# Optimization experiments

Measured on AMD Instinct MI355X. Metric: run time of the kernel, lower is better.

## Reference

```python
import jax, jax.numpy as jnp
import numpy as np

C = 256
N, H, W = 4, 64, 64


def _conv1x1(x, w, b):
    # 1x1 Conv2d == per-pixel linear: x [N,C,H,W], w [O,C], b [O]
    return jnp.einsum('nchw,oc->nohw', x, w) + b[None, :, None, None]


def setup_inputs() -> dict:
    key = jax.random.key(0)
    ks = jax.random.split(key, 9)
    inputs = jax.random.normal(ks[0], (N, C, H, W), dtype=jnp.float32)
    scale = 1.0 / np.sqrt(C)
    d = {'inputs': inputs}
    for i in range(4):
        d[f'w{i}'] = jax.random.normal(ks[1 + 2 * i], (C, C), dtype=jnp.float32) * scale
        d[f'b{i}'] = jax.random.normal(ks[2 + 2 * i], (C,), dtype=jnp.float32) * 0.01
    return d


def reference(inputs, w0, b0, w1, b1, w2, b2, w3, b3):
    n, c, h, w = inputs.shape
    hw = h * w
    # f_v, f_k, f_q: [N, HW, C] (NCHW conv output permuted to NHWC then flattened)
    f_v = _conv1x1(inputs, w0, b0).transpose(0, 2, 3, 1).reshape(n, hw, c)
    f_k = _conv1x1(inputs, w1, b1).transpose(0, 2, 3, 1).reshape(n, hw, c)
    f_q = _conv1x1(inputs, w2, b2).transpose(0, 2, 3, 1).reshape(n, hw, c)
    # w[n,i,j] = <k_i, q_j> / HW   (no softmax)
    att = jnp.einsum('nid,njd->nij', f_k, f_q) / hw
    # f_r[n,j,c] = sum_i w[n,i,j] * v[n,i,c]  (matmul with w^T)
    f_r = jnp.einsum('nij,nic->njc', att, f_v)
    f_r = f_r.reshape(n, h, w, c).transpose(0, 3, 1, 2)  # back to NCHW
    return _conv1x1(f_r, w3, b3)
```

## Files before the change

### kernel.cpp

```cpp
#include <hip/hip_runtime.h>

#define NB 4
#define CD 256
#define HW 4096
#define KSG 16
#define CC (CD * CD)

typedef __attribute__((ext_vector_type(8))) short bf16x8;
typedef __attribute__((ext_vector_type(4))) float f32x4;

__device__ inline unsigned short f2bf(float x) {
  unsigned int u = __float_as_uint(x);
  unsigned int r = (u + 0x7FFFu + ((u >> 16) & 1u)) >> 16;
  return (unsigned short)r;
}
__device__ inline float bfhi(unsigned short h) {
  return __uint_as_float(((unsigned int)h) << 16);
}
__device__ __forceinline__ void gload16(const unsigned short* g, unsigned short* l) {
  __builtin_amdgcn_global_load_lds((const __attribute__((address_space(1))) void*)g,
                                   (__attribute__((address_space(3))) void*)l, 16, 0, 0);
}

template <int BOFF>
__device__ __forceinline__ void mfma_body(const unsigned short* sm, f32x4 acc[4][2]) {
  int t = threadIdx.x, lane = t & 63, wid = t >> 6;
  int wr = wid >> 2, wc = wid & 3;
  int lrow = lane & 15, lkb = lane >> 4;
#pragma unroll
  for (int ks2 = 0; ks2 < 2; ++ks2) {
    bf16x8 ah[4], al[4], bh[2], bl[2];
#pragma unroll
    for (int m = 0; m < 4; ++m) {
      int r = wr * 64 + m * 16 + lrow;
      int sw = ((ks2 * 4 + lkb) ^ (r & 7)) * 8;
      ah[m] = *(const bf16x8*)(sm + r * 64 + sw);
      al[m] = *(const bf16x8*)(sm + 8192 + r * 64 + sw);
    }
#pragma unroll
    for (int q = 0; q < 2; ++q) {
      int r = wc * 32 + q * 16 + lrow;
      int sw = ((ks2 * 4 + lkb) ^ (r & 7)) * 8;
      bh[q] = *(const bf16x8*)(sm + BOFF + r * 64 + sw);
      bl[q] = *(const bf16x8*)(sm + BOFF + 8192 + r * 64 + sw);
    }
#pragma unroll
    for (int m = 0; m < 4; ++m)
#pragma unroll
      for (int q = 0; q < 2; ++q) {
        acc[m][q] = __builtin_amdgcn_mfma_f32_16x16x32_bf16(ah[m], bh[q], acc[m][q], 0, 0, 0);
        acc[m][q] = __builtin_amdgcn_mfma_f32_16x16x32_bf16(ah[m], bl[q], acc[m][q], 0, 0, 0);
        acc[m][q] = __builtin_amdgcn_mfma_f32_16x16x32_bf16(al[m], bh[q], acc[m][q], 0, 0, 0);
      }
  }
}

__device__ __forceinline__ void mfma_nt_core(
    const unsigned short* __restrict__ pH, const unsigned short* __restrict__ pL,
    const unsigned short* __restrict__ qH, const unsigned short* __restrict__ qL,
    int i0, int j0, unsigned short* sm, f32x4 acc[4][2]) {
  int t = threadIdx.x;
  int lane = t & 63, wid = t >> 6;
  int tsel = wid >> 1;
  int gbase = (wid & 1) * 8;
  const unsigned short* bp2 = (tsel == 0) ? pH : (tsel == 1) ? pL : (tsel == 2) ? qH : qL;
  int tb = (tsel < 2) ? i0 : j0;
  int rsub = lane >> 3;
  int gc = (lane & 7) ^ rsub;
  unsigned short* ldsT = sm + tsel * 8192;
#pragma unroll
  for (int m = 0; m < 4; ++m)
#pragma unroll
    for (int q = 0; q < 2; ++q) acc[m][q] = (f32x4){0.f, 0.f, 0.f, 0.f};
  for (int k0 = 0; k0 < 256; k0 += 64) {
#pragma unroll
    for (int s = 0; s < 8; ++s) {
      int g = gbase + s;
      gload16(bp2 + (size_t)(tb + g * 8 + rsub) * CD + k0 + gc * 8, ldsT + g * 512);
    }
    __syncthreads();
    mfma_body<16384>(sm, acc);
    __syncthreads();
  }
}

template <bool DIAG, int NSTEP>
__device__ __forceinline__ void gram_core(const float* __restrict__ Xn, int i0, int j0,
                                          int kBegin, unsigned short* sm,
                                          f32x4 acc[4][2], float* __restrict__ psumRow) {
  int t = threadIdx.x;
  int r16 = t >> 4, k4 = (t & 15) * 4;
  int kg = k4 >> 3, kr = k4 & 7;
#pragma unroll
  for (int m = 0; m < 4; ++m)
#pragma unroll
    for (int q = 0; q < 2; ++q) acc[m][q] = (f32x4){0.f, 0.f, 0.f, 0.f};
  float ps[4] = {0.f, 0.f, 0.f, 0.f};
  float4 av[4], bv[4];
#pragma unroll
  for (int j = 0; j < 4; ++j) {
    av[j] = *(const float4*)(Xn + (size_t)(i0 + j * 32 + r16) * HW + kBegin + k4);
    if (!DIAG)
      bv[j] = *(const float4*)(Xn + (size_t)(j0 + j * 32 + r16) * HW + kBegin + k4);
  }
#pragma unroll
  for (int s = 0; s < NSTEP; ++s) {
    float4 av2[4], bv2[4];
    if (s < NSTEP - 1) {
#pragma unroll
      for (int j = 0; j < 4; ++j) {
        av2[j] = *(const float4*)(Xn + (size_t)(i0 + j * 32 + r16) * HW + kBegin +
                                  (s + 1) * 64 + k4);
        if (!DIAG)
          bv2[j] = *(const float4*)(Xn + (size_t)(j0 + j * 32 + r16) * HW + kBegin +
                                    (s + 1) * 64 + k4);
      }
    }
#pragma unroll
    for (int j = 0; j < 4; ++j) {
      int r = j * 32 + r16;
      int off = r * 64 + ((kg ^ (r & 7)) << 3) + kr;
      ushort4 h, l;
      h.x = f2bf(av[j].x); l.x = f2bf(av[j].x - bfhi(h.x));
      h.y = f2bf(av[j].y); l.y = f2bf(av[j].y - bfhi(h.y));
      h.z = f2bf(av[j].z); l.z = f2bf(av[j].z - bfhi(h.z));
      h.w = f2bf(av[j].w); l.w = f2bf(av[j].w - bfhi(h.w));
      *(ushort4*)(sm + off) = h;
      *(ushort4*)(sm + 8192 + off) = l;
      ps[j] += av[j].x + av[j].y + av[j].z + av[j].w;
      if (!DIAG) {
        h.x = f2bf(bv[j].x); l.x = f2bf(bv[j].x - bfhi(h.x));
        h.y = f2bf(bv[j].y); l.y = f2bf(bv[j].y - bfhi(h.y));
        h.z = f2bf(bv[j].z); l.z = f2bf(bv[j].z - bfhi(h.z));
        h.w = f2bf(bv[j].w); l.w = f2bf(bv[j].w - bfhi(h.w));
        *(ushort4*)(sm + 16384 + off) = h;
        *(ushort4*)(sm + 24576 + off) = l;
      }
    }
    __syncthreads();
    mfma_body<DIAG ? 0 : 16384>(sm, acc);
    __syncthreads();
    if (s < NSTEP - 1) {
#pragma unroll
      for (int j = 0; j < 4; ++j) {
        av[j] = av2[j];
        if (!DIAG) bv[j] = bv2[j];
      }
    }
  }
  if (psumRow) {
#pragma unroll
    for (int j = 0; j < 4; ++j) {
      float v = ps[j];
      v += __shfl_xor(v, 1); v += __shfl_xor(v, 2);
      v += __shfl_xor(v, 4); v += __shfl_xor(v, 8);
      if ((t & 15) == 0) psumRow[j * 32 + r16] = v;
    }
  }
}

__device__ __forceinline__ void stage_rowA(const float* __restrict__ W, int ld, int r0,
                                           int k0, unsigned short* dst) {
  int t = threadIdx.x;
  int r16 = t >> 4, k4 = (t & 15) * 4;
  int kg = k4 >> 3, kr = k4 & 7;
#pragma unroll
  for (int j = 0; j < 4; ++j) {
    int r = j * 32 + r16;
    float4 v = *(const float4*)(W + (size_t)(r0 + r) * ld + k0 + k4);
    int off = r * 64 + ((kg ^ (r & 7)) << 3) + kr;
    ushort4 h, l;
    h.x = f2bf(v.x); l.x = f2bf(v.x - bfhi(h.x));
    h.y = f2bf(v.y); l.y = f2bf(v.y - bfhi(h.y));
    h.z = f2bf(v.z); l.z = f2bf(v.z - bfhi(h.z));
    h.w = f2bf(v.w); l.w = f2bf(v.w - bfhi(h.w));
    *(ushort4*)(dst + off) = h;
    *(ushort4*)(dst + 8192 + off) = l;
  }
}

__device__ __forceinline__ void stage_colT(const float* __restrict__ W, int ld, int c0,
                                           int k0, unsigned short* dst) {
  int t = threadIdx.x;
#pragma unroll
  for (int ee = 0; ee < 8; ++ee) {
    int flat = ee * 512 + t;
    int c2 = flat >> 7, p = flat & 127;
    const float* src = W + (size_t)(k0 + 2 * c2) * ld + c0 + p;
    float xa = src[0], xb = src[ld];
    int c = 2 * c2;
    int off = p * 64 + ((((c >> 3)) ^ (p & 7)) << 3) + (c & 7);
    unsigned short ha = f2bf(xa), hb = f2bf(xb);
    ushort2 hv; hv.x = ha; hv.y = hb;
    ushort2 lv; lv.x = f2bf(xa - bfhi(ha)); lv.y = f2bf(xb - bfhi(hb));
    *(ushort2*)(dst + off) = hv;
    *(ushort2*)(dst + 8192 + off) = lv;
  }
}

__device__ __forceinline__ void mfma_body64(const unsigned short* sm, f32x4 acc[4]) {
  int t = threadIdx.x, lane = t & 63, wid = t >> 6;
  int wr = wid >> 2, wc = wid & 3;
  int lrow = lane & 15, lkb = lane >> 4;
#pragma unroll
  for (int ks2 = 0; ks2 < 2; ++ks2) {
    bf16x8 ah[4], al[4], bh, bl;
#pragma unroll
    for (int m = 0; m < 4; ++m) {
      int r = wr * 64 + m * 16 + lrow;
      int sw = ((ks2 * 4 + lkb) ^ (r & 7)) * 8;
      ah[m] = *(const bf16x8*)(sm + r * 64 + sw);
      al[m] = *(const bf16x8*)(sm + 8192 + r * 64 + sw);
    }
    {
      int r = wc * 16 + lrow;
      int sw = ((ks2 * 4 + lkb) ^ (r & 7)) * 8;
      bh = *(const bf16x8*)(sm + 16384 + r * 64 + sw);
      bl = *(const bf16x8*)(sm + 20480 + r * 64 + sw);
    }
#pragma unroll
    for (int m = 0; m < 4; ++m) {
      acc[m] = __builtin_amdgcn_mfma_f32_16x16x32_bf16(ah[m], bh, acc[m], 0, 0, 0);
      acc[m] = __builtin_amdgcn_mfma_f32_16x16x32_bf16(ah[m], bl, acc[m], 0, 0, 0);
      acc[m] = __builtin_amdgcn_mfma_f32_16x16x32_bf16(al[m], bh, acc[m], 0, 0, 0);
    }
  }
}

__device__ __forceinline__ void final_core64(const unsigned short* __restrict__ aH,
                                             const unsigned short* __restrict__ aL,
                                             const float* __restrict__ Xn, int i0, int j0,
                                             unsigned short* sm, f32x4 acc[4]) {
  int t = threadIdx.x, lane = t & 63, wid = t >> 6;
  const unsigned short* ap = (wid & 4) ? aL : aH;
  unsigned short* ldsA = sm + ((wid & 4) ? 8192 : 0);
  int rsub = lane >> 3;
  int gc = (lane & 7) ^ rsub;
  int gq = wid & 3;
#pragma unroll
  for (int m = 0; m < 4; ++m) acc[m] = (f32x4){0.f, 0.f, 0.f, 0.f};
  float xa[4], xb[4];
#pragma unroll
  for (int s2 = 0; s2 < 4; ++s2) {
    int g = gq * 4 + s2;
    gload16(ap + (size_t)(i0 + g * 8 + rsub) * CD + gc * 8, ldsA + g * 512);
  }
#pragma unroll
  for (int ee = 0; ee < 4; ++ee) {
    int flat = ee * 512 + t;
    int c2 = flat >> 6, p = flat & 63;
    const float* src = Xn + (size_t)(2 * c2) * HW + j0 + p;
    xa[ee] = src[0];
    xb[ee] = src[HW];
  }
#pragma unroll
  for (int s = 0; s < 4; ++s) {
#pragma unroll
    for (int ee = 0; ee < 4; ++ee) {
      int flat = ee * 512 + t;
      int c2 = flat >> 6, p = flat & 63;
      int c = 2 * c2;
      int off = p * 64 + ((((c >> 3)) ^ (p & 7)) << 3) + (c & 7);
      unsigned short ha = f2bf(xa[ee]), hb = f2bf(xb[ee]);
      ushort2 hv; hv.x = ha; hv.y = hb;
      ushort2 lv; lv.x = f2bf(xa[ee] - bfhi(ha)); lv.y = f2bf(xb[ee] - bfhi(hb));
      *(ushort2*)(sm + 16384 + off) = hv;
      *(ushort2*)(sm + 20480 + off) = lv;
    }
    float xa2[4], xb2[4];
    if (s < 3) {
#pragma unroll
      for (int ee = 0; ee < 4; ++ee) {
        int flat = ee * 512 + t;
        int c2 = flat >> 6, p = flat & 63;
        const float* src = Xn + (size_t)((s + 1) * 64 + 2 * c2) * HW + j0 + p;
        xa2[ee] = src[0];
        xb2[ee] = src[HW];
      }
    }
    __syncthreads();
    mfma_body64(sm, acc);
    __syncthreads();
    if (s < 3) {
#pragma unroll
      for (int s2 = 0; s2 < 4; ++s2) {
        int g = gq * 4 + s2;
        gload16(ap + (size_t)(i0 + g * 8 + rsub) * CD + (s + 1) * 64 + gc * 8,
                ldsA + g * 512);
      }
#pragma unroll
      for (int ee = 0; ee < 4; ++ee) { xa[ee] = xa2[ee]; xb[ee] = xb2[ee]; }
    }
  }
}

__device__ __forceinline__ void epi_store(f32x4 acc[4][2], float* smf, float* dst,
                                          int ld, const float* cvrow) {
  int t = threadIdx.x, lane = t & 63, wid = t >> 6;
  int wr = wid >> 2, wc = wid & 3;
#pragma unroll
  for (int m = 0; m < 4; ++m) {
    int rbase = wr * 64 + m * 16 + ((lane >> 4) << 2);
#pragma unroll
    for (int q = 0; q < 2; ++q) {
      int col = wc * 32 + q * 16 + (lane & 15);
#pragma unroll
      for (int e = 0; e < 4; ++e) {
        int row = rbase + e;
        smf[row * 128 + (col ^ ((row & 4) << 2))] = acc[m][q][e];
      }
    }
  }
  __syncthreads();
#pragma unroll
  for (int it = 0; it < 8; ++it) {
    int row = it * 16 + wid * 2 + (lane >> 5);
    int col = (lane & 31) * 4;
    float4 v = *(const float4*)&smf[row * 128 + (col ^ ((row & 4) << 2))];
    if (cvrow) {
      float cb = cvrow[row];
      v.x += cb; v.y += cb; v.z += cb; v.w += cb;
    }
    *(float4*)(dst + (size_t)row * ld + col) = v;
  }
}

__device__ __forceinline__ void epi_store64(f32x4 acc[4], float* smf, float* dst,
                                            const float* cvrow) {
  int t = threadIdx.x, lane = t & 63, wid = t >> 6;
  int wr = wid >> 2, wc = wid & 3;
#pragma unroll
  for (int m = 0; m < 4; ++m) {
    int rbase = wr * 64 + m * 16 + ((lane >> 4) << 2);
    int col = wc * 16 + (lane & 15);
#pragma unroll
    for (int e = 0; e < 4; ++e) {
      int row = rbase + e;
      smf[row * 64 + (col ^ ((row & 4) << 2))] = acc[m][e];
    }
  }
  __syncthreads();
#pragma unroll
  for (int it = 0; it < 4; ++it) {
    int slot = it * 512 + t;
    int row = slot >> 4, col = (slot & 15) * 4;
    float4 v = *(const float4*)&smf[row * 64 + (col ^ ((row & 4) << 2))];
    float cb = cvrow[row];
    v.x += cb; v.y += cb; v.z += cb; v.w += cb;
    *(float4*)(dst + (size_t)row * HW + col) = v;
  }
}

__global__ __launch_bounds__(512) void kB(
    const float* __restrict__ X, float* __restrict__ Gp, float* __restrict__ psum2,
    const float* __restrict__ w0, const float* __restrict__ w1,
    const float* __restrict__ w2, const float* __restrict__ w3,
    const float* __restrict__ b0, const float* __restrict__ b1,
    const float* __restrict__ b2, unsigned short* __restrict__ Eh,
    unsigned short* __restrict__ El, float* __restrict__ Et,
    unsigned short* __restrict__ Fth, unsigned short* __restrict__ Ftl,
    float* __restrict__ Ff, float* __restrict__ vp, float* __restrict__ bpv,
    float* __restrict__ dlt, float* __restrict__ scal1) {
  __shared__ __align__(16) unsigned short sm[32768];
  int x = blockIdx.x, t = threadIdx.x;
  if (x < 192) {
    int tile = x % 3;
    int z = x / 3;
    int n = z >> 4, ks = z & 15;
    const float* Xn = X + (size_t)n * CD * HW;
    f32x4 acc[4][2];
    if (tile == 1) {
      gram_core<false, 4>(Xn, 0, 128, ks * 256, sm, acc, nullptr);
      epi_store(acc, (float*)sm, Gp + ((size_t)ks * NB + n) * CC + 128, CD, nullptr);
    } else {
      int i0 = (tile == 2) ? 128 : 0;
      float* psRow = psum2 + ((size_t)n * KSG + ks) * 256 + i0;
      gram_core<true, 4>(Xn, i0, i0, ks * 256, sm, acc, psRow);
      epi_store(acc, (float*)sm,
                Gp + ((size_t)ks * NB + n) * CC + (size_t)i0 * CD + i0, CD, nullptr);
    }
  } else if (x < 200) {
    int e = x - 192;
    int zc = e >> 2, q = e & 3;
    int i0 = (q >> 1) * 128, j0 = (q & 1) * 128;
    f32x4 acc[4][2];
#pragma unroll
    for (int m = 0; m < 4; ++m)
#pragma unroll
      for (int qq = 0; qq < 2; ++qq) acc[m][qq] = (f32x4){0.f, 0.f, 0.f, 0.f};
    for (int s = 0; s < 4; ++s) {
      int k0 = s * 64;
      if (zc == 0) stage_rowA(w3, CD, i0, k0, sm);
      else stage_colT(w2, CD, i0, k0, sm);
      stage_colT(zc ? w1 : w0, CD, j0, k0, sm + 16384);
      __syncthreads();
      mfma_body<16384>(sm, acc);
      __syncthreads();
    }
    unsigned short* oh = zc ? Fth : Eh;
    unsigned short* ol = zc ? Ftl : El;
    float* tf = zc ? Ff : Et;
    int lane = t & 63, wid = t >> 6, wr = wid >> 2, wc = wid & 3;
#pragma unroll
    for (int m = 0; m < 4; ++m) {
      int row = i0 + wr * 64 + m * 16 + ((lane >> 4) << 2);
#pragma unroll
      for (int q2 = 0; q2 < 2; ++q2) {
        int col = j0 + wc * 32 + q2 * 16 + (lane & 15);
#pragma unroll
        for (int e2 = 0; e2 < 4; ++e2) {
          float v = acc[m][q2][e2];
          unsigned short hh = f2bf(v), ll = f2bf(v - bfhi(hh));
          oh[(size_t)(row + e2) * CD + col] = hh;
          ol[(size_t)(row + e2) * CD + col] = ll;
          tf[(size_t)col * CD + row + e2] = v;
        }
      }
    }
  } else {
    int task = x - 200;
    if (task < 8) {
      float* vin = (float*)sm;
      int seg = task & 3;
      const float* Wm = (task < 4) ? w1 : w2;
      const float* v = (task < 4) ? b2 : b1;
      float* dst = (task < 4) ? (vp + seg * CD) : (bpv + seg * CD);
      if (t < 64) vin[t] = v[seg * 64 + t];
      __syncthreads();
      if (t < 256) {
        float a = 0.f;
#pragma unroll 16
        for (int kk = 0; kk < 64; ++kk)
          a += Wm[(size_t)(seg * 64 + kk) * CD + t] * vin[kk];
        dst[t] = a;
      }
    } else if (task < 12) {
      int lane = t & 63, wv = t >> 6;
      float4 bvv = *(const float4*)(b0 + lane * 4);
#pragma unroll
      for (int i = 0; i < 8; ++i) {
        int o = (task - 8) * 64 + wv * 8 + i;
        float4 v = *(const float4*)(w3 + (size_t)o * CD + lane * 4);
        float a = v.x * bvv.x + v.y * bvv.y + v.z * bvv.z + v.w * bvv.w;
        a += __shfl_xor(a, 1);  a += __shfl_xor(a, 2);  a += __shfl_xor(a, 4);
        a += __shfl_xor(a, 8);  a += __shfl_xor(a, 16); a += __shfl_xor(a, 32);
        if (lane == 0) dlt[o] = a;
      }
    } else if (task == 12) {
      float* red = (float*)sm;
      if (t < 256) red[t] = b1[t] * b2[t];
      __syncthreads();
      for (int off = 128; off > 0; off >>= 1) {
        if (t < off) red[t] += red[t + off];
        __syncthreads();
      }
      if (t == 0) scal1[0] = red[0];
    }
  }
}

__global__ __launch_bounds__(512) void kC(
    const float* __restrict__ Gp, unsigned short* __restrict__ Gh,
    unsigned short* __restrict__ Gl, const float* __restrict__ psum2,
    const float* __restrict__ vp, const float* __restrict__ Ff,
    const float* __restrict__ Et, float* __restrict__ alp, float* __restrict__ gam,
    float* __restrict__ scal0) {
  __shared__ float smf[512];
  int b = blockIdx.x, t = threadIdx.x;
  if (b < 96) {
#pragma unroll
    for (int s = 0; s < 4; ++s) {
      int f = b * 2048 + s * 512 + t;
      int b2 = f >> 8, tt = f & 255;
      int quad = b2 >> 8, r = b2 & 255, n = r >> 6;
      int idx = (r & 63) * 256 + tt;
      int i = (idx >> 7) + ((quad == 2) ? 128 : 0);
      int j = (idx & 127) + ((quad >= 1) ? 128 : 0);
      float a = 0.f;
#pragma unroll
      for (int ks = 0; ks < KSG; ++ks)
        a += Gp[((size_t)ks * NB + n) * CC + (size_t)i * CD + j];
      size_t o = (size_t)n * CC + (size_t)i * CD + j;
      unsigned short hh = f2bf(a), ll = f2bf(a - bfhi(hh));
      Gh[o] = hh; Gl[o] = ll;
      if (quad == 1) {
        size_t o2 = (size_t)n * CC + (size_t)j * CD + i;
        Gh[o2] = hh; Gl[o2] = ll;
      }
    }
  } else {
    int n = b - 96;
    float* ss = smf;
    float* red = ss + 256;
    float a = 0.f;
    if (t < 256) {
#pragma unroll
      for (int ks = 0; ks < KSG; ++ks) a += psum2[((size_t)n * KSG + ks) * 256 + t];
      ss[t] = a;
      red[t] = a * (vp[t] + vp[CD + t] + vp[2 * CD + t] + vp[3 * CD + t]);
    }
    __syncthreads();
    for (int off = 128; off > 0; off >>= 1) {
      if (t < off) red[t] += red[t + off];
      __syncthreads();
    }
    if (t == 0) scal0[n] = red[0];
    if (t < 256) {
      float al = 0.f, ga = 0.f;
#pragma unroll 16
      for (int k = 0; k < CD; ++k) {
        float sk = ss[k];
        al += Ff[(size_t)k * CD + t] * sk;
        ga += Et[(size_t)k * CD + t] * sk;
      }
      alp[n * CD + t] = al;
      gam[n * CD + t] = ga;
    }
  }
}

__global__ __launch_bounds__(512) void kD1(
    const unsigned short* __restrict__ Eh, const unsigned short* __restrict__ El,
    const unsigned short* __restrict__ Gh, const unsigned short* __restrict__ Gl,
    unsigned short* __restrict__ Rh, unsigned short* __restrict__ Rl,
    const float* __restrict__ Et, const float* __restrict__ vp,
    const float* __restrict__ dlt, const float* __restrict__ gam,
    const float* __restrict__ scal0, const float* __restrict__ scal1,
    const float* __restrict__ b3, float* __restrict__ cv) {
  __shared__ __align__(16) unsigned short sm[32768];
  int b = blockIdx.x, t = threadIdx.x;
  if (b < 16) {
    int n = b >> 2, i0 = ((b >> 1) & 1) * 128, j0 = (b & 1) * 128;
    f32x4 acc[4][2];
    mfma_nt_core(Eh, El, Gh + (size_t)n * CC, Gl + (size_t)n * CC, i0, j0, sm, acc);
    int lane = t & 63, wid = t >> 6, wr = wid >> 2, wc = wid & 3;
#pragma unroll
    for (int m = 0; m < 4; ++m) {
      int row = i0 + wr * 64 + m * 16 + ((lane >> 4) << 2);
#pragma unroll
      for (int q = 0; q < 2; ++q) {
        int col = j0 + wc * 32 + q * 16 + (lane & 15);
#pragma unroll
        for (int e = 0; e < 4; ++e) {
          float v = acc[m][q][e];
          unsigned short hh = f2bf(v), ll = f2bf(v - bfhi(hh));
          Rh[(size_t)n * CC + (size_t)(row + e) * CD + col] = hh;
          Rl[(size_t)n * CC + (size_t)(row + e) * CD + col] = ll;
        }
      }
    }
  } else {
    int n = b - 16;
    float* vsh = (float*)sm;
    float* g1 = vsh + CD;
    if (t < CD) vsh[t] = vp[t] + vp[CD + t] + vp[2 * CD + t] + vp[3 * CD + t];
    __syncthreads();
    if (t < CD) {
      const unsigned short* GhN = Gh + (size_t)n * CC;
      const unsigned short* GlN = Gl + (size_t)n * CC;
      float a = 0.f;
#pragma unroll 8
      for (int k = 0; k < CD; ++k) {
        float g = bfhi(GhN[(size_t)k * CD + t]) + bfhi(GlN[(size_t)k * CD + t]);
        a += g * vsh[k];
      }
      g1[t] = a;
    }
    __syncthreads();
    if (t < CD) {
      float c2 = 0.f;
#pragma unroll 8
      for (int k = 0; k < CD; ++k) c2 += Et[(size_t)k * CD + t] * g1[k];
      cv[n * CD + t] = (c2 + scal0[n] * dlt[t] +
                        scal1[0] * (gam[n * CD + t] + (float)HW * dlt[t])) *
                           (1.0f / HW) +
                       b3[t];
    }
  }
}

__global__ __launch_bounds__(512) void kD2(
    const unsigned short* __restrict__ Rh, const unsigned short* __restrict__ Rl,
    const unsigned short* __restrict__ Fth, const unsigned short* __restrict__ Ftl,
    unsigned short* __restrict__ Athi, unsigned short* __restrict__ Atlo,
    const float* __restrict__ dlt, const float* __restrict__ alp,
    const float* __restrict__ gam, const float* __restrict__ bpv) {
  __shared__ __align__(16) unsigned short sm[32768];
  int b = blockIdx.x, t = threadIdx.x;
  int n = b >> 2, i0 = ((b >> 1) & 1) * 128, j0 = (b & 1) * 128;
  f32x4 acc[4][2];
  mfma_nt_core(Rh + (size_t)n * CC, Rl + (size_t)n * CC, Fth, Ftl, i0, j0, sm, acc);
  int lane = t & 63, wid = t >> 6, wr = wid >> 2, wc = wid & 3;
#pragma unroll
  for (int m = 0; m < 4; ++m) {
    int row = i0 + wr * 64 + m * 16 + ((lane >> 4) << 2);
#pragma unroll
    for (int q = 0; q < 2; ++q) {
      int col = j0 + wc * 32 + q * 16 + (lane & 15);
      float bj = bpv[col] + bpv[CD + col] + bpv[2 * CD + col] + bpv[3 * CD + col];
      float aj = alp[n * CD + col];
#pragma unroll
      for (int e = 0; e < 4; ++e) {
        float di = dlt[row + e], gi = gam[n * CD + row + e];
        float v = (acc[m][q][e] + di * aj + gi * bj) * (1.0f / HW) + di * bj;
        unsigned short hh = f2bf(v), ll = f2bf(v - bfhi(hh));
        Athi[(size_t)n * CC + (size_t)(row + e) * CD + col] = hh;
        Atlo[(size_t)n * CC + (size_t)(row + e) * CD + col] = ll;
      }
    }
  }
}

__global__ __launch_bounds__(512) void kF(const unsigned short* __restrict__ Athi,
                                          const unsigned short* __restrict__ Atlo,
                                          const float* __restrict__ X,
                                          const float* __restrict__ cv,
                                          float* __restrict__ out) {
  int n = blockIdx.y;
  int x = blockIdx.x;
  int i0 = (x & 1) * 128;
  int j0 = (x >> 1) * 64;
  __shared__ __align__(16) unsigned short sm[24576];
  f32x4 acc[4];
  final_core64(Athi + (size_t)n * CC, Atlo + (size_t)n * CC, X + (size_t)n * CD * HW,
               i0, j0, sm, acc);
  epi_store64(acc, (float*)sm, out + (size_t)n * CD * HW + (size_t)i0 * HW + j0,
              cv + n * CD + i0);
}

extern "C" void kernel_launch(void* const* d_in, const int* in_sizes, int n_in,
                              void* d_out, int out_size, void* d_ws, size_t ws_size,
                              hipStream_t stream) {
  const float* X = (const float*)d_in[0];
  const float* w0 = (const float*)d_in[1];
  const float* b0 = (const float*)d_in[2];
  const float* w1 = (const float*)d_in[3];
  const float* b1 = (const float*)d_in[4];
  const float* w2 = (const float*)d_in[5];
  const float* b2 = (const float*)d_in[6];
  const float* w3 = (const float*)d_in[7];
  const float* b3 = (const float*)d_in[8];
  float* out = (float*)d_out;
  float* ws = (float*)d_ws;

  float* cv    = ws;
  float* alp   = ws + 1024;
  float* gam   = ws + 2048;
  float* dlt   = ws + 3072;
  float* vp    = ws + 4096;
  float* bpv   = ws + 5120;
  float* scal0 = ws + 6144;
  float* scal1 = ws + 6176;
  float* psum2 = ws + 8192;
  float* Et    = psum2 + 16384;
  float* Ff    = Et + CC;
  float* Gp    = Ff + CC;
  unsigned short* Eh   = (unsigned short*)(Gp + (size_t)KSG * NB * CC);
  unsigned short* El   = Eh + CC;
  unsigned short* Fth  = El + CC;
  unsigned short* Ftl  = Fth + CC;
  unsigned short* Gh   = Ftl + CC;
  unsigned short* Gl   = Gh + (size_t)NB * CC;
  unsigned short* Rh   = Gl + (size_t)NB * CC;
  unsigned short* Rl   = Rh + (size_t)NB * CC;
  unsigned short* Athi = Rl + (size_t)NB * CC;
  unsigned short* Atlo = Athi + (size_t)NB * CC;

  kB<<<dim3(213), 512, 0, stream>>>(X, Gp, psum2, w0, w1, w2, w3, b0, b1, b2, Eh, El,
                                    Et, Fth, Ftl, Ff, vp, bpv, dlt, scal1);
  kC<<<dim3(100), 512, 0, stream>>>(Gp, Gh, Gl, psum2, vp, Ff, Et, alp, gam, scal0);
  kD1<<<dim3(20), 512, 0, stream>>>(Eh, El, Gh, Gl, Rh, Rl, Et, vp, dlt, gam, scal0,
                                    scal1, b3, cv);
  kD2<<<dim3(16), 512, 0, stream>>>(Rh, Rl, Fth, Ftl, Athi, Atlo, dlt, alp, gam, bpv);
  kF<<<dim3(128, NB), 512, 0, stream>>>(Athi, Atlo, X, cv, out);
}
```

Before: 74.87 us.

## Fuse the two chained 256x256 GEMM kernels into one, keeping the intermediate in LDS

Merges kD1 (R = E·G) and kD2 (A = R·Ft plus epilogue) into a single kernel kD. Each block computes a 64-row strip of R across all 256 columns, stores it as split bf16 hi/lo in shared memory, then multiplies it by Ft for its 128-column output tile. This removes one kernel launch and the global write and reread of the R intermediate. In exchange, R is recomputed redundantly for each column half, and the larger LDS footprint (about 112 KB) limits occupancy on the 36-block launch.

```diff
diff --git a/kernel.cpp b/kernel.cpp
--- a/kernel.cpp
+++ b/kernel.cpp
@@ -52,35 +52,6 @@
         acc[m][q] = __builtin_amdgcn_mfma_f32_16x16x32_bf16(ah[m], bl[q], acc[m][q], 0, 0, 0);
         acc[m][q] = __builtin_amdgcn_mfma_f32_16x16x32_bf16(al[m], bh[q], acc[m][q], 0, 0, 0);
       }
-  }
-}
-
-__device__ __forceinline__ void mfma_nt_core(
-    const unsigned short* __restrict__ pH, const unsigned short* __restrict__ pL,
-    const unsigned short* __restrict__ qH, const unsigned short* __restrict__ qL,
-    int i0, int j0, unsigned short* sm, f32x4 acc[4][2]) {
-  int t = threadIdx.x;
-  int lane = t & 63, wid = t >> 6;
-  int tsel = wid >> 1;
-  int gbase = (wid & 1) * 8;
-  const unsigned short* bp2 = (tsel == 0) ? pH : (tsel == 1) ? pL : (tsel == 2) ? qH : qL;
-  int tb = (tsel < 2) ? i0 : j0;
-  int rsub = lane >> 3;
-  int gc = (lane & 7) ^ rsub;
-  unsigned short* ldsT = sm + tsel * 8192;
-#pragma unroll
-  for (int m = 0; m < 4; ++m)
-#pragma unroll
-    for (int q = 0; q < 2; ++q) acc[m][q] = (f32x4){0.f, 0.f, 0.f, 0.f};
-  for (int k0 = 0; k0 < 256; k0 += 64) {
-#pragma unroll
-    for (int s = 0; s < 8; ++s) {
-      int g = gbase + s;
-      gload16(bp2 + (size_t)(tb + g * 8 + rsub) * CD + k0 + gc * 8, ldsT + g * 512);
-    }
-    __syncthreads();
-    mfma_body<16384>(sm, acc);
-    __syncthreads();
   }
 }
 
@@ -519,38 +490,199 @@
   }
 }
 
-__global__ __launch_bounds__(512) void kD1(
+__global__ __launch_bounds__(512) void kD(
     const unsigned short* __restrict__ Eh, const unsigned short* __restrict__ El,
     const unsigned short* __restrict__ Gh, const unsigned short* __restrict__ Gl,
-    unsigned short* __restrict__ Rh, unsigned short* __restrict__ Rl,
+    const unsigned short* __restrict__ Fth, const unsigned short* __restrict__ Ftl,
+    unsigned short* __restrict__ Athi, unsigned short* __restrict__ Atlo,
+    const float* __restrict__ dlt, const float* __restrict__ alp,
+    const float* __restrict__ gam, const float* __restrict__ bpv,
     const float* __restrict__ Et, const float* __restrict__ vp,
-    const float* __restrict__ dlt, const float* __restrict__ gam,
     const float* __restrict__ scal0, const float* __restrict__ scal1,
     const float* __restrict__ b3, float* __restrict__ cv) {
-  __shared__ __align__(16) unsigned short sm[32768];
+  __shared__ __align__(16) unsigned short sm[57344];
   int b = blockIdx.x, t = threadIdx.x;
-  if (b < 16) {
-    int n = b >> 2, i0 = ((b >> 1) & 1) * 128, j0 = (b & 1) * 128;
-    f32x4 acc[4][2];
-    mfma_nt_core(Eh, El, Gh + (size_t)n * CC, Gl + (size_t)n * CC, i0, j0, sm, acc);
-    int lane = t & 63, wid = t >> 6, wr = wid >> 2, wc = wid & 3;
-#pragma unroll
-    for (int m = 0; m < 4; ++m) {
-      int row = i0 + wr * 64 + m * 16 + ((lane >> 4) << 2);
+  if (b < 32) {
+    int n = b >> 3, i0 = ((b >> 1) & 3) * 64, j0 = (b & 1) * 128;
+    int lane = t & 63, wid = t >> 6;
+    int wr = wid >> 2, wc = wid & 3;
+    int lrow = lane & 15, lkb = lane >> 4;
+    int rsub = lane >> 3, gcx = (lane & 7) ^ rsub;
+    const unsigned short* GhN = Gh + (size_t)n * CC;
+    const unsigned short* GlN = Gl + (size_t)n * CC;
+    f32x4 acc1[2][2][2];
+#pragma unroll
+    for (int m = 0; m < 2; ++m)
+#pragma unroll
+      for (int h = 0; h < 2; ++h)
+#pragma unroll
+        for (int q = 0; q < 2; ++q) acc1[m][h][q] = (f32x4){0.f, 0.f, 0.f, 0.f};
+    for (int k0 = 0; k0 < 256; k0 += 64) {
+#pragma unroll
+      for (int u = 0; u < 6; ++u) {
+        int flat = wid * 6 + u;
+        if (flat < 8)
+          gload16(Eh + (size_t)(i0 + flat * 8 + rsub) * CD + k0 + gcx * 8, sm + flat * 512);
+        else if (flat < 16)
+          gload16(El + (size_t)(i0 + (flat - 8) * 8 + rsub) * CD + k0 + gcx * 8,
+                  sm + 4096 + (flat - 8) * 512);
+        else if (flat < 32)
+          gload16(GhN + (size_t)((flat - 16) * 8 + rsub) * CD + k0 + gcx * 8,
+                  sm + 8192 + (flat - 16) * 512);
+        else
+          gload16(GlN + (size_t)((flat - 32) * 8 + rsub) * CD + k0 + gcx * 8,
+                  sm + 16384 + (flat - 32) * 512);
+      }
+      __syncthreads();
+#pragma unroll
+      for (int ks2 = 0; ks2 < 2; ++ks2) {
+        bf16x8 ah[2], al[2], bh[2], bl[2];
+#pragma unroll
+        for (int m = 0; m < 2; ++m) {
+          int r = wr * 32 + m * 16 + lrow;
+          int sw = ((ks2 * 4 + lkb) ^ (r & 7)) * 8;
+          ah[m] = *(const bf16x8*)(sm + r * 64 + sw);
+          al[m] = *(const bf16x8*)(sm + 4096 + r * 64 + sw);
+        }
+#pragma unroll
+        for (int q = 0; q < 2; ++q) {
+          int rr = wc * 32 + q * 16 + lrow;
+          int sw = ((ks2 * 4 + lkb) ^ (rr & 7)) * 8;
+          bh[q] = *(const bf16x8*)(sm + 8192 + rr * 64 + sw);
+          bl[q] = *(const bf16x8*)(sm + 16384 + rr * 64 + sw);
+        }
+#pragma unroll
+        for (int m = 0; m < 2; ++m)
+#pragma unroll
+          for (int q = 0; q < 2; ++q) {
+            acc1[m][0][q] = __builtin_amdgcn_mfma_f32_16x16x32_bf16(ah[m], bh[q], acc1[m][0][q], 0, 0, 0);
+            acc1[m][0][q] = __builtin_amdgcn_mfma_f32_16x16x32_bf16(ah[m], bl[q], acc1[m][0][q], 0, 0, 0);
+            acc1[m][0][q] = __builtin_amdgcn_mfma_f32_16x16x32_bf16(al[m], bh[q], acc1[m][0][q], 0, 0, 0);
+          }
+      }
+      __syncthreads();
+#pragma unroll
+      for (int u = 0; u < 4; ++u) {
+        int flat = wid * 4 + u;
+        if (flat < 16)
+          gload16(GhN + (size_t)(128 + flat * 8 + rsub) * CD + k0 + gcx * 8,
+                  sm + 8192 + flat * 512);
+        else
+          gload16(GlN + (size_t)(128 + (flat - 16) * 8 + rsub) * CD + k0 + gcx * 8,
+                  sm + 16384 + (flat - 16) * 512);
+      }
+      __syncthreads();
+#pragma unroll
+      for (int ks2 = 0; ks2 < 2; ++ks2) {
+        bf16x8 ah[2], al[2], bh[2], bl[2];
+#pragma unroll
+        for (int m = 0; m < 2; ++m) {
+          int r = wr * 32 + m * 16 + lrow;
+          int sw = ((ks2 * 4 + lkb) ^ (r & 7)) * 8;
+          ah[m] = *(const bf16x8*)(sm + r * 64 + sw);
+          al[m] = *(const bf16x8*)(sm + 4096 + r * 64 + sw);
+        }
+#pragma unroll
+        for (int q = 0; q < 2; ++q) {
+          int rr = wc * 32 + q * 16 + lrow;
+          int sw = ((ks2 * 4 + lkb) ^ (rr & 7)) * 8;
+          bh[q] = *(const bf16x8*)(sm + 8192 + rr * 64 + sw);
+          bl[q] = *(const bf16x8*)(sm + 16384 + rr * 64 + sw);
+        }
+#pragma unroll
+        for (int m = 0; m < 2; ++m)
+#pragma unroll
+          for (int q = 0; q < 2; ++q) {
+            acc1[m][1][q] = __builtin_amdgcn_mfma_f32_16x16x32_bf16(ah[m], bh[q], acc1[m][1][q], 0, 0, 0);
+            acc1[m][1][q] = __builtin_amdgcn_mfma_f32_16x16x32_bf16(ah[m], bl[q], acc1[m][1][q], 0, 0, 0);
+            acc1[m][1][q] = __builtin_amdgcn_mfma_f32_16x16x32_bf16(al[m], bh[q], acc1[m][1][q], 0, 0, 0);
+          }
+      }
+      __syncthreads();
+    }
+#pragma unroll
+    for (int m = 0; m < 2; ++m)
+#pragma unroll
+      for (int h = 0; h < 2; ++h)
+#pragma unroll
+        for (int q = 0; q < 2; ++q)
+#pragma unroll
+          for (int e = 0; e < 4; ++e) {
+            int row = wr * 32 + m * 16 + ((lane >> 4) << 2) + e;
+            int col = h * 128 + wc * 32 + q * 16 + (lane & 15);
+            float v = acc1[m][h][q][e];
+            unsigned short hh = f2bf(v), ll = f2bf(v - bfhi(hh));
+            int c = col >> 6, ccv = col & 63;
+            int off = c * 4096 + row * 64 + (((ccv >> 3) ^ (row & 7)) << 3) + (ccv & 7);
+            sm[24576 + off] = hh;
+            sm[40960 + off] = ll;
+          }
+    __syncthreads();
+    f32x4 acc2[2][2];
+#pragma unroll
+    for (int m = 0; m < 2; ++m)
+#pragma unroll
+      for (int q = 0; q < 2; ++q) acc2[m][q] = (f32x4){0.f, 0.f, 0.f, 0.f};
+    for (int c = 0; c < 4; ++c) {
+#pragma unroll
+      for (int u = 0; u < 4; ++u) {
+        int flat = wid * 4 + u;
+        if (flat < 16)
+          gload16(Fth + (size_t)(j0 + flat * 8 + rsub) * CD + c * 64 + gcx * 8,
+                  sm + 8192 + flat * 512);
+        else
+          gload16(Ftl + (size_t)(j0 + (flat - 16) * 8 + rsub) * CD + c * 64 + gcx * 8,
+                  sm + 16384 + (flat - 16) * 512);
+      }
+      __syncthreads();
+#pragma unroll
+      for (int ks2 = 0; ks2 < 2; ++ks2) {
+        bf16x8 ah[2], al[2], bh[2], bl[2];
+#pragma unroll
+        for (int m = 0; m < 2; ++m) {
+          int r = wr * 32 + m * 16 + lrow;
+          int sw = ((ks2 * 4 + lkb) ^ (r & 7)) * 8;
+          ah[m] = *(const bf16x8*)(sm + 24576 + c * 4096 + r * 64 + sw);
+          al[m] = *(const bf16x8*)(sm + 40960 + c * 4096 + r * 64 + sw);
+        }
+#pragma unroll
+        for (int q = 0; q < 2; ++q) {
+          int rr = wc * 32 + q * 16 + lrow;
+          int sw = ((ks2 * 4 + lkb) ^ (rr & 7)) * 8;
+          bh[q] = *(const bf16x8*)(sm + 8192 + rr * 64 + sw);
+          bl[q] = *(const bf16x8*)(sm + 16384 + rr * 64 + sw);
+        }
+#pragma unroll
+        for (int m = 0; m < 2; ++m)
+#pragma unroll
+          for (int q = 0; q < 2; ++q) {
+            acc2[m][q] = __builtin_amdgcn_mfma_f32_16x16x32_bf16(ah[m], bh[q], acc2[m][q], 0, 0, 0);
+            acc2[m][q] = __builtin_amdgcn_mfma_f32_16x16x32_bf16(ah[m], bl[q], acc2[m][q], 0, 0, 0);
+            acc2[m][q] = __builtin_amdgcn_mfma_f32_16x16x32_bf16(al[m], bh[q], acc2[m][q], 0, 0, 0);
+          }
+      }
+      __syncthreads();
+    }
+#pragma unroll
+    for (int m = 0; m < 2; ++m) {
+      int row = i0 + wr * 32 + m * 16 + ((lane >> 4) << 2);
 #pragma unroll
       for (int q = 0; q < 2; ++q) {
         int col = j0 + wc * 32 + q * 16 + (lane & 15);
+        float bj = bpv[col] + bpv[CD + col] + bpv[2 * CD + col] + bpv[3 * CD + col];
+        float aj = alp[n * CD + col];
 #pragma unroll
         for (int e = 0; e < 4; ++e) {
-          float v = acc[m][q][e];
+          float di = dlt[row + e], gi = gam[n * CD + row + e];
+          float v = (acc2[m][q][e] + di * aj + gi * bj) * (1.0f / HW) + di * bj;
           unsigned short hh = f2bf(v), ll = f2bf(v - bfhi(hh));
-          Rh[(size_t)n * CC + (size_t)(row + e) * CD + col] = hh;
-          Rl[(size_t)n * CC + (size_t)(row + e) * CD + col] = ll;
+          Athi[(size_t)n * CC + (size_t)(row + e) * CD + col] = hh;
+          Atlo[(size_t)n * CC + (size_t)(row + e) * CD + col] = ll;
         }
       }
     }
   } else {
-    int n = b - 16;
+    int n = b - 32;
     float* vsh = (float*)sm;
     float* g1 = vsh + CD;
     if (t < CD) vsh[t] = vp[t] + vp[CD + t] + vp[2 * CD + t] + vp[3 * CD + t];
@@ -575,38 +707,6 @@
                         scal1[0] * (gam[n * CD + t] + (float)HW * dlt[t])) *
                            (1.0f / HW) +
                        b3[t];
-    }
-  }
-}
-
-__global__ __launch_bounds__(512) void kD2(
-    const unsigned short* __restrict__ Rh, const unsigned short* __restrict__ Rl,
-    const unsigned short* __restrict__ Fth, const unsigned short* __restrict__ Ftl,
-    unsigned short* __restrict__ Athi, unsigned short* __restrict__ Atlo,
-    const float* __restrict__ dlt, const float* __restrict__ alp,
-    const float* __restrict__ gam, const float* __restrict__ bpv) {
-  __shared__ __align__(16) unsigned short sm[32768];
-  int b = blockIdx.x, t = threadIdx.x;
-  int n = b >> 2, i0 = ((b >> 1) & 1) * 128, j0 = (b & 1) * 128;
-  f32x4 acc[4][2];
-  mfma_nt_core(Rh + (size_t)n * CC, Rl + (size_t)n * CC, Fth, Ftl, i0, j0, sm, acc);
-  int lane = t & 63, wid = t >> 6, wr = wid >> 2, wc = wid & 3;
-#pragma unroll
-  for (int m = 0; m < 4; ++m) {
-    int row = i0 + wr * 64 + m * 16 + ((lane >> 4) << 2);
-#pragma unroll
-    for (int q = 0; q < 2; ++q) {
-      int col = j0 + wc * 32 + q * 16 + (lane & 15);
-      float bj = bpv[col] + bpv[CD + col] + bpv[2 * CD + col] + bpv[3 * CD + col];
-      float aj = alp[n * CD + col];
-#pragma unroll
-      for (int e = 0; e < 4; ++e) {
-        float di = dlt[row + e], gi = gam[n * CD + row + e];
-        float v = (acc[m][q][e] + di * aj + gi * bj) * (1.0f / HW) + di * bj;
-        unsigned short hh = f2bf(v), ll = f2bf(v - bfhi(hh));
-        Athi[(size_t)n * CC + (size_t)(row + e) * CD + col] = hh;
-        Atlo[(size_t)n * CC + (size_t)(row + e) * CD + col] = ll;
-      }
     }
   }
 }
@@ -661,16 +761,13 @@
   unsigned short* Ftl  = Fth + CC;
   unsigned short* Gh   = Ftl + CC;
   unsigned short* Gl   = Gh + (size_t)NB * CC;
-  unsigned short* Rh   = Gl + (size_t)NB * CC;
-  unsigned short* Rl   = Rh + (size_t)NB * CC;
-  unsigned short* Athi = Rl + (size_t)NB * CC;
+  unsigned short* Athi = Gl + (size_t)NB * CC;
   unsigned short* Atlo = Athi + (size_t)NB * CC;
 
   kB<<<dim3(213), 512, 0, stream>>>(X, Gp, psum2, w0, w1, w2, w3, b0, b1, b2, Eh, El,
                                     Et, Fth, Ftl, Ff, vp, bpv, dlt, scal1);
   kC<<<dim3(100), 512, 0, stream>>>(Gp, Gh, Gl, psum2, vp, Ff, Et, alp, gam, scal0);
-  kD1<<<dim3(20), 512, 0, stream>>>(Eh, El, Gh, Gl, Rh, Rl, Et, vp, dlt, gam, scal0,
-                                    scal1, b3, cv);
-  kD2<<<dim3(16), 512, 0, stream>>>(Rh, Rl, Fth, Ftl, Athi, Atlo, dlt, alp, gam, bpv);
+  kD<<<dim3(36), 512, 0, stream>>>(Eh, El, Gh, Gl, Fth, Ftl, Athi, Atlo, dlt, alp, gam,
+                                   bpv, Et, vp, scal0, scal1, b3, cv);
   kF<<<dim3(128, NB), 512, 0, stream>>>(Athi, Atlo, X, cv, out);
 }
```

New measurement: 63.91 us (median of 3 runs). -14.6%, faster.
